# Optimization experiments

Hardware: AMD Instinct MI355X
Metric: run time of the kernel (lower is better)

## Reference

```python
import jax, jax.numpy as jnp
import numpy as np

H = 1024       # hidden_size
V = 32000      # output_vocab_size
STEPS = 375    # fixed greedy decode length in the original loop


def setup_inputs() -> dict:
    key = jax.random.key(0)
    ks = jax.random.split(key, 6)
    s = 0.02  # init scale
    return {
        "encoder_hidden": jax.random.normal(ks[0], (1, 1, H), dtype=jnp.float32),
        "emb": jax.random.normal(ks[1], (V, H), dtype=jnp.float32) * s,
        "W_ih": jax.random.normal(ks[2], (3 * H, H), dtype=jnp.float32) * s,   # [W_ir;W_iz;W_in]
        "W_hh": jax.random.normal(ks[3], (3 * H, H), dtype=jnp.float32) * s,   # [W_hr;W_hz;W_hn]
        "b_ih": jnp.zeros((3 * H,), dtype=jnp.float32),
        "b_hh": jnp.zeros((3 * H,), dtype=jnp.float32),
        "lin_W": jax.random.normal(ks[4], (V, H), dtype=jnp.float32) * s,
        "lin_b": jnp.zeros((V,), dtype=jnp.float32),
    }


def _gru_cell(x, h, W_ih, W_hh, b_ih, b_hh):
    # PyTorch GRU gate math (gate order r, z, n)
    gi = W_ih @ x + b_ih            # [3H]
    gh = W_hh @ h + b_hh            # [3H]
    i_r, i_z, i_n = jnp.split(gi, 3)
    h_r, h_z, h_n = jnp.split(gh, 3)
    r = jax.nn.sigmoid(i_r + h_r)
    z = jax.nn.sigmoid(i_z + h_z)
    n = jnp.tanh(i_n + r * h_n)
    return (1.0 - z) * n + z * h


def reference(encoder_hidden, emb, W_ih, W_hh, b_ih, b_hh, lin_W, lin_b):
    h0 = encoder_hidden[0, 0]  # [H], batch=1, single layer

    def step(carry, _):
        h, tok = carry
        x = emb[tok]                                   # embedding lookup [H]
        h_new = _gru_cell(x, h, W_ih, W_hh, b_ih, b_hh)
        logits = lin_W @ h_new + lin_b                 # [V]
        logp = jax.nn.log_softmax(logits)              # LogSoftmax(dim=1) on [1,V]
        next_tok = jnp.argmax(logp).astype(jnp.int32)  # greedy feedback
        return (h_new, next_tok), logp

    (h_final, _), outs = jax.lax.scan(
        step, (h0, jnp.int32(0)), None, length=STEPS)
    # original cats [1,V] outputs along dim 0 -> [STEPS, V]
    return outs, h_final.reshape(1, 1, H)
```

## Files before the change

kernel.cpp:

```cpp
#include <hip/hip_runtime.h>

#define H 1024
#define V 32000
#define STEPS 375
#define NB1 256
#define NB2 512

typedef float vfloat4 __attribute__((ext_vector_type(4)));

__device__ __forceinline__ float dot4(const float4 a, const float4 b) {
    return fmaf(a.x, b.x, fmaf(a.y, b.y, fmaf(a.z, b.z, a.w * b.w)));
}

__device__ __forceinline__ float wave_sum(float v) {
#pragma unroll
    for (int off = 32; off > 0; off >>= 1) v += __shfl_xor(v, off);
    return v;
}

__device__ __forceinline__ void sm_merge(float& m, float& ss, int& a,
                                         float om, float os, int oa) {
    if (om > m || (om == m && oa < a)) {
        ss = os + ss * expf(m - om); m = om; a = oa;
    } else {
        ss += os * expf(om - m);
    }
}

__device__ __forceinline__ void load_row4(const float4* p, int lane, float4 w[4], bool nt) {
    if (nt) {
        const vfloat4* q = (const vfloat4*)p;
#pragma unroll
        for (int j = 0; j < 4; ++j) {
            vfloat4 t = __builtin_nontemporal_load(&q[lane + 64 * j]);
            w[j] = make_float4(t.x, t.y, t.z, t.w);
        }
    } else {
#pragma unroll
        for (int j = 0; j < 4; ++j) w[j] = p[lane + 64 * j];
    }
}

__global__ void init_kernel(const float* __restrict__ enc, float* __restrict__ h0) {
    for (int i = threadIdx.x; i < H; i += 256) h0[i] = enc[i];
}

__global__ __launch_bounds__(256) void gru_kernel(
    const float* __restrict__ emb, const float* __restrict__ W_ih,
    const float* __restrict__ W_hh, const float* __restrict__ b_ih,
    const float* __restrict__ b_hh, const float* __restrict__ h_cur,
    float* __restrict__ h_next, float* __restrict__ logz,
    const float* __restrict__ pm, const float* __restrict__ ps,
    const int* __restrict__ pa, int s) {
    const int tid = threadIdx.x;
    const int lane = tid & 63;
    const int wv = tid >> 6;
    const int b = blockIdx.x;

    int tok = 0;
    if (s > 0) {
        float m = -3.4e38f, ss = 0.f;
        int a = 0x7fffffff;
#pragma unroll
        for (int k = 0; k < NB2 / 64; ++k)
            sm_merge(m, ss, a, pm[k * 64 + lane], ps[k * 64 + lane], pa[k * 64 + lane]);
#pragma unroll
        for (int off = 32; off > 0; off >>= 1) {
            float om = __shfl_xor(m, off), os = __shfl_xor(ss, off);
            int oa = __shfl_xor(a, off);
            sm_merge(m, ss, a, om, os, oa);
        }
        tok = a;
        if (b == 0 && tid == 0) logz[s - 1] = m + logf(ss);
    }

    const int i = b * 4 + wv;
    const float4* xp = (const float4*)(emb + (size_t)tok * H);
    const float4* hp = (const float4*)h_cur;
    float4 xv[4], hv[4];
#pragma unroll
    for (int j = 0; j < 4; ++j) {
        xv[j] = xp[lane + 64 * j];
        hv[j] = hp[lane + 64 * j];
    }
    float4 WX0[4], WX1[4], WX2[4], WH0[4], WH1[4], WH2[4];
    load_row4((const float4*)(W_ih + (size_t)i * H), lane, WX0, false);
    load_row4((const float4*)(W_ih + ((size_t)i + H) * H), lane, WX1, false);
    load_row4((const float4*)(W_ih + ((size_t)i + 2 * H) * H), lane, WX2, false);
    load_row4((const float4*)(W_hh + (size_t)i * H), lane, WH0, false);
    load_row4((const float4*)(W_hh + ((size_t)i + H) * H), lane, WH1, false);
    load_row4((const float4*)(W_hh + ((size_t)i + 2 * H) * H), lane, WH2, false);
    float sx0 = 0, sx1 = 0, sx2 = 0, sh0 = 0, sh1 = 0, sh2 = 0;
#pragma unroll
    for (int j = 0; j < 4; ++j) {
        sx0 += dot4(WX0[j], xv[j]); sx1 += dot4(WX1[j], xv[j]); sx2 += dot4(WX2[j], xv[j]);
        sh0 += dot4(WH0[j], hv[j]); sh1 += dot4(WH1[j], hv[j]); sh2 += dot4(WH2[j], hv[j]);
    }
    sx0 = wave_sum(sx0); sx1 = wave_sum(sx1); sx2 = wave_sum(sx2);
    sh0 = wave_sum(sh0); sh1 = wave_sum(sh1); sh2 = wave_sum(sh2);
    if (lane == 0) {
        const float rg = 1.f / (1.f + expf(-((sx0 + b_ih[i]) + (sh0 + b_hh[i]))));
        const float zg = 1.f / (1.f + expf(-((sx1 + b_ih[i + H]) + (sh1 + b_hh[i + H]))));
        const float ng = tanhf((sx2 + b_ih[i + 2 * H]) + rg * (sh2 + b_hh[i + 2 * H]));
        h_next[i] = (1.f - zg) * ng + zg * h_cur[i];
    }
}

__global__ __launch_bounds__(512, 4) void logits_kernel(
    const float* __restrict__ lin_W, const float* __restrict__ lin_b,
    const float* __restrict__ h_src, float* __restrict__ orow,
    float* __restrict__ pm, float* __restrict__ ps, int* __restrict__ pa) {
    const int tid = threadIdx.x;
    const int lane = tid & 63;
    const int wv = tid >> 6;
    const int b = blockIdx.x;
    const int row0 = (b < 256) ? 63 * b : 16128 + 62 * (b - 256);
    const int nrows = (b < 256) ? 63 : 62;
    const bool nt = (wv == 3) || (wv == 7);

    __shared__ float red_m[8], red_s[8];
    __shared__ int red_a[8];

    const float4* h4 = (const float4*)h_src;
    float4 hr[4];
#pragma unroll
    for (int j = 0; j < 4; ++j) hr[j] = h4[lane + 64 * j];

    float m = -3.4e38f, ssum = 0.f;
    int arg = 0x7fffffff;
    for (int r = wv; r < nrows; r += 32) {
        const int rB = r + 8, rC = r + 16, rD = r + 24;
        const bool vB = rB < nrows, vC = rC < nrows, vD = rD < nrows;
        float4 wA[4], wB[4], wC[4], wD[4];
        load_row4((const float4*)(lin_W + (size_t)(row0 + r) * H), lane, wA, nt);
        load_row4((const float4*)(lin_W + (size_t)(row0 + (vB ? rB : r)) * H), lane, wB, nt);
        load_row4((const float4*)(lin_W + (size_t)(row0 + (vC ? rC : r)) * H), lane, wC, nt);
        load_row4((const float4*)(lin_W + (size_t)(row0 + (vD ? rD : r)) * H), lane, wD, nt);
        __builtin_amdgcn_sched_barrier(0);
        float aA = 0, aB = 0, aC = 0, aD = 0;
#pragma unroll
        for (int j = 0; j < 4; ++j) {
            aA += dot4(wA[j], hr[j]); aB += dot4(wB[j], hr[j]);
            aC += dot4(wC[j], hr[j]); aD += dot4(wD[j], hr[j]);
        }
        aA = wave_sum(aA); aB = wave_sum(aB);
        aC = wave_sum(aC); aD = wave_sum(aD);
        aA += lin_b[row0 + r];
        if (lane == 0) __builtin_nontemporal_store(aA, &orow[row0 + r]);
        if (aA > m) { ssum *= expf(m - aA); m = aA; arg = row0 + r; }
        ssum += expf(aA - m);
        if (vB) {
            aB += lin_b[row0 + rB];
            if (lane == 0) __builtin_nontemporal_store(aB, &orow[row0 + rB]);
            if (aB > m) { ssum *= expf(m - aB); m = aB; arg = row0 + rB; }
            ssum += expf(aB - m);
        }
        if (vC) {
            aC += lin_b[row0 + rC];
            if (lane == 0) __builtin_nontemporal_store(aC, &orow[row0 + rC]);
            if (aC > m) { ssum *= expf(m - aC); m = aC; arg = row0 + rC; }
            ssum += expf(aC - m);
        }
        if (vD) {
            aD += lin_b[row0 + rD];
            if (lane == 0) __builtin_nontemporal_store(aD, &orow[row0 + rD]);
            if (aD > m) { ssum *= expf(m - aD); m = aD; arg = row0 + rD; }
            ssum += expf(aD - m);
        }
    }
    if (lane == 0) { red_m[wv] = m; red_s[wv] = ssum; red_a[wv] = arg; }
    __syncthreads();
    if (tid == 0) {
        float M = red_m[0], S = red_s[0];
        int A = red_a[0];
#pragma unroll
        for (int w = 1; w < 8; ++w) sm_merge(M, S, A, red_m[w], red_s[w], red_a[w]);
        pm[b] = M; ps[b] = S; pa[b] = A;
    }
}

__global__ __launch_bounds__(256) void final_kernel(float* __restrict__ out,
                                                    const float* __restrict__ logz) {
    const int row = blockIdx.x >> 3;
    const int seg = blockIdx.x & 7;
    const float lz = logz[row];
    float4* p = (float4*)(out + (size_t)row * V) + seg * 1000;
    for (int i = threadIdx.x; i < 1000; i += 256) {
        float4 v = p[i];
        v.x -= lz; v.y -= lz; v.z -= lz; v.w -= lz;
        p[i] = v;
    }
}

__global__ __launch_bounds__(256) void tail_kernel(
    float* __restrict__ out_last, const float* __restrict__ pm,
    const float* __restrict__ ps, const int* __restrict__ pa,
    const float* __restrict__ h_final, float* __restrict__ out_h) {
    const int tid = threadIdx.x;
    const int lane = tid & 63;
    const int b = blockIdx.x;
    float m = -3.4e38f, ss = 0.f;
    int a = 0x7fffffff;
#pragma unroll
    for (int k = 0; k < NB2 / 64; ++k)
        sm_merge(m, ss, a, pm[k * 64 + lane], ps[k * 64 + lane], pa[k * 64 + lane]);
#pragma unroll
    for (int off = 32; off > 0; off >>= 1) {
        float om = __shfl_xor(m, off), os = __shfl_xor(ss, off);
        int oa = __shfl_xor(a, off);
        sm_merge(m, ss, a, om, os, oa);
    }
    const float logZ = m + logf(ss);
    if (tid < 125) out_last[b * 125 + tid] -= logZ;
    if (b == 0)
        for (int i = tid; i < H; i += 256) out_h[i] = h_final[i];
}

extern "C" void kernel_launch(void* const* d_in, const int* in_sizes, int n_in,
                              void* d_out, int out_size, void* d_ws, size_t ws_size,
                              hipStream_t stream) {
    const float* enc = (const float*)d_in[0];
    const float* emb = (const float*)d_in[1];
    const float* W_ih = (const float*)d_in[2];
    const float* W_hh = (const float*)d_in[3];
    const float* b_ih = (const float*)d_in[4];
    const float* b_hh = (const float*)d_in[5];
    const float* lin_W = (const float*)d_in[6];
    const float* lin_b = (const float*)d_in[7];
    float* out = (float*)d_out;
    float* ws = (float*)d_ws;

    float* h_buf = ws;
    float* pm = ws + 2 * H;
    float* ps = pm + NB2;
    int* pa = (int*)(ps + NB2);
    float* logz = (float*)(pa + NB2);

    init_kernel<<<1, 256, 0, stream>>>(enc, h_buf);
    for (int s = 0; s < STEPS; ++s) {
        float* h_cur = h_buf + (s & 1) * H;
        float* h_next = h_buf + ((s + 1) & 1) * H;
        gru_kernel<<<NB1, 256, 0, stream>>>(emb, W_ih, W_hh, b_ih, b_hh,
                                            h_cur, h_next, logz, pm, ps, pa, s);
        logits_kernel<<<NB2, 512, 0, stream>>>(lin_W, lin_b, h_next,
                                               out + (size_t)s * V, pm, ps, pa);
    }
    final_kernel<<<(STEPS - 1) * 8, 256, 0, stream>>>(out, logz);
    tail_kernel<<<NB1, 256, 0, stream>>>(out + (size_t)(STEPS - 1) * V, pm, ps, pa,
                                         h_buf + (STEPS & 1) * H,
                                         out + (size_t)V * STEPS);
}
```

Baseline: 13.02 ms.

## Stream bf16 copy of output projection, recheck near-max rows in fp32

```diff
diff --git a/kernel.cpp b/kernel.cpp
--- a/kernel.cpp
+++ b/kernel.cpp
@@ -5,8 +5,7 @@
 #define STEPS 375
 #define NB1 256
 #define NB2 512
-
-typedef float vfloat4 __attribute__((ext_vector_type(4)));
+#define DELTA 0.25f
 
 __device__ __forceinline__ float dot4(const float4 a, const float4 b) {
     return fmaf(a.x, b.x, fmaf(a.y, b.y, fmaf(a.z, b.z, a.w * b.w)));
@@ -27,22 +26,29 @@
     }
 }
 
-__device__ __forceinline__ void load_row4(const float4* p, int lane, float4 w[4], bool nt) {
-    if (nt) {
-        const vfloat4* q = (const vfloat4*)p;
-#pragma unroll
-        for (int j = 0; j < 4; ++j) {
-            vfloat4 t = __builtin_nontemporal_load(&q[lane + 64 * j]);
-            w[j] = make_float4(t.x, t.y, t.z, t.w);
-        }
-    } else {
-#pragma unroll
-        for (int j = 0; j < 4; ++j) w[j] = p[lane + 64 * j];
-    }
+__device__ __forceinline__ float bl(unsigned u) { return __uint_as_float(u << 16); }
+__device__ __forceinline__ float bh(unsigned u) { return __uint_as_float(u & 0xffff0000u); }
+
+__device__ __forceinline__ unsigned f2bf(float f) {
+    unsigned u = __float_as_uint(f);
+    return (u + 0x7fffu + ((u >> 16) & 1u)) >> 16;
 }
 
 __global__ void init_kernel(const float* __restrict__ enc, float* __restrict__ h0) {
     for (int i = threadIdx.x; i < H; i += 256) h0[i] = enc[i];
+}
+
+__global__ __launch_bounds__(512) void conv_kernel(const float* __restrict__ src,
+                                                   unsigned short* __restrict__ dst) {
+    const size_t idx = (size_t)blockIdx.x * 512 + threadIdx.x;
+    const float4* s4 = (const float4*)src;
+    float4 a = s4[2 * idx], b = s4[2 * idx + 1];
+    uint4 o;
+    o.x = f2bf(a.x) | (f2bf(a.y) << 16);
+    o.y = f2bf(a.z) | (f2bf(a.w) << 16);
+    o.z = f2bf(b.x) | (f2bf(b.y) << 16);
+    o.w = f2bf(b.z) | (f2bf(b.w) << 16);
+    ((uint4*)dst)[idx] = o;
 }
 
 __global__ __launch_bounds__(256) void gru_kernel(
@@ -56,6 +62,22 @@
     const int lane = tid & 63;
     const int wv = tid >> 6;
     const int b = blockIdx.x;
+    const int i = b * 4 + wv;
+
+    const float4* hp = (const float4*)h_cur;
+    float4 hv[4];
+    float4 WX0[4], WX1[4], WX2[4], WH0[4], WH1[4], WH2[4];
+#pragma unroll
+    for (int j = 0; j < 4; ++j) {
+        const int idx = lane + 64 * j;
+        hv[j] = hp[idx];
+        WX0[j] = ((const float4*)(W_ih + (size_t)i * H))[idx];
+        WX1[j] = ((const float4*)(W_ih + ((size_t)i + H) * H))[idx];
+        WX2[j] = ((const float4*)(W_ih + ((size_t)i + 2 * H) * H))[idx];
+        WH0[j] = ((const float4*)(W_hh + (size_t)i * H))[idx];
+        WH1[j] = ((const float4*)(W_hh + ((size_t)i + H) * H))[idx];
+        WH2[j] = ((const float4*)(W_hh + ((size_t)i + 2 * H) * H))[idx];
+    }
 
     int tok = 0;
     if (s > 0) {
@@ -74,22 +96,11 @@
         if (b == 0 && tid == 0) logz[s - 1] = m + logf(ss);
     }
 
-    const int i = b * 4 + wv;
     const float4* xp = (const float4*)(emb + (size_t)tok * H);
-    const float4* hp = (const float4*)h_cur;
-    float4 xv[4], hv[4];
-#pragma unroll
-    for (int j = 0; j < 4; ++j) {
-        xv[j] = xp[lane + 64 * j];
-        hv[j] = hp[lane + 64 * j];
-    }
-    float4 WX0[4], WX1[4], WX2[4], WH0[4], WH1[4], WH2[4];
-    load_row4((const float4*)(W_ih + (size_t)i * H), lane, WX0, false);
-    load_row4((const float4*)(W_ih + ((size_t)i + H) * H), lane, WX1, false);
-    load_row4((const float4*)(W_ih + ((size_t)i + 2 * H) * H), lane, WX2, false);
-    load_row4((const float4*)(W_hh + (size_t)i * H), lane, WH0, false);
-    load_row4((const float4*)(W_hh + ((size_t)i + H) * H), lane, WH1, false);
-    load_row4((const float4*)(W_hh + ((size_t)i + 2 * H) * H), lane, WH2, false);
+    float4 xv[4];
+#pragma unroll
+    for (int j = 0; j < 4; ++j) xv[j] = xp[lane + 64 * j];
+
     float sx0 = 0, sx1 = 0, sx2 = 0, sh0 = 0, sh1 = 0, sh2 = 0;
 #pragma unroll
     for (int j = 0; j < 4; ++j) {
@@ -106,7 +117,120 @@
     }
 }
 
-__global__ __launch_bounds__(512, 4) void logits_kernel(
+__global__ __launch_bounds__(512, 4) void logits_bf16_kernel(
+    const unsigned short* __restrict__ wbf, const float* __restrict__ lin_W,
+    const float* __restrict__ lin_b, const float* __restrict__ h_src,
+    float* __restrict__ orow, float* __restrict__ pm, float* __restrict__ ps,
+    int* __restrict__ pa) {
+    const int tid = threadIdx.x;
+    const int lane = tid & 63;
+    const int wv = tid >> 6;
+    const int b = blockIdx.x;
+    const int row0 = (b < 256) ? 63 * b : 16128 + 62 * (b - 256);
+    const int nrows = (b < 256) ? 63 : 62;
+
+    __shared__ float red_m[8], red_s[8];
+    __shared__ float s_cm[8];
+    __shared__ int s_ca[8];
+
+    const float4* h4 = (const float4*)h_src;
+    const float4 ha0 = h4[2 * lane], ha1 = h4[2 * lane + 1];
+    const float4 hb0 = h4[128 + 2 * lane], hb1 = h4[129 + 2 * lane];
+    const float h0[8] = {ha0.x, ha0.y, ha0.z, ha0.w, ha1.x, ha1.y, ha1.z, ha1.w};
+    const float h1[8] = {hb0.x, hb0.y, hb0.z, hb0.w, hb1.x, hb1.y, hb1.z, hb1.w};
+
+    float lg[8];
+    float m = -3.4e38f, ssum = 0.f;
+
+#pragma unroll
+    for (int half = 0; half < 2; ++half) {
+        const int k0 = half * 4;
+        uint4 qa[4], qb[4];
+        int rr[4];
+        bool val[4];
+#pragma unroll
+        for (int i2 = 0; i2 < 4; ++i2) {
+            rr[i2] = wv + 8 * (k0 + i2);
+            val[i2] = rr[i2] < nrows;
+            const uint4* wp = (const uint4*)(wbf + (size_t)(row0 + (val[i2] ? rr[i2] : 0)) * H);
+            qa[i2] = wp[lane];
+            qb[i2] = wp[64 + lane];
+        }
+        __builtin_amdgcn_sched_barrier(0);
+#pragma unroll
+        for (int i2 = 0; i2 < 4; ++i2) {
+            float a = 0.f;
+            a = fmaf(bl(qa[i2].x), h0[0], a); a = fmaf(bh(qa[i2].x), h0[1], a);
+            a = fmaf(bl(qa[i2].y), h0[2], a); a = fmaf(bh(qa[i2].y), h0[3], a);
+            a = fmaf(bl(qa[i2].z), h0[4], a); a = fmaf(bh(qa[i2].z), h0[5], a);
+            a = fmaf(bl(qa[i2].w), h0[6], a); a = fmaf(bh(qa[i2].w), h0[7], a);
+            a = fmaf(bl(qb[i2].x), h1[0], a); a = fmaf(bh(qb[i2].x), h1[1], a);
+            a = fmaf(bl(qb[i2].y), h1[2], a); a = fmaf(bh(qb[i2].y), h1[3], a);
+            a = fmaf(bl(qb[i2].z), h1[4], a); a = fmaf(bh(qb[i2].z), h1[5], a);
+            a = fmaf(bl(qb[i2].w), h1[6], a); a = fmaf(bh(qb[i2].w), h1[7], a);
+            a = wave_sum(a);
+            if (val[i2]) {
+                const int col = row0 + rr[i2];
+                a += lin_b[col];
+                lg[k0 + i2] = a;
+                if (lane == 0) __builtin_nontemporal_store(a, &orow[col]);
+                if (a > m) { ssum *= expf(m - a); m = a; }
+                ssum += expf(a - m);
+            } else {
+                lg[k0 + i2] = -3.4e38f;
+            }
+        }
+    }
+    if (lane == 0) { red_m[wv] = m; red_s[wv] = ssum; }
+    __syncthreads();
+
+    float Mb = red_m[0];
+#pragma unroll
+    for (int w = 1; w < 8; ++w) Mb = fmaxf(Mb, red_m[w]);
+
+    float cm = -3.4e38f;
+    int ca = 0x7fffffff;
+    float4 hv[4];
+    bool loaded = false;
+#pragma unroll
+    for (int k = 0; k < 8; ++k) {
+        if (lg[k] > Mb - DELTA) {
+            const int row = row0 + wv + 8 * k;
+            if (!loaded) {
+#pragma unroll
+                for (int j = 0; j < 4; ++j) hv[j] = h4[lane + 64 * j];
+                loaded = true;
+            }
+            const float4* rp = (const float4*)(lin_W + (size_t)row * H);
+            float a = 0.f;
+#pragma unroll
+            for (int j = 0; j < 4; ++j) a += dot4(rp[lane + 64 * j], hv[j]);
+            a = wave_sum(a) + lin_b[row];
+            if (a > cm || (a == cm && row < ca)) { cm = a; ca = row; }
+        }
+    }
+    if (lane == 0) { s_cm[wv] = cm; s_ca[wv] = ca; }
+    __syncthreads();
+    if (tid == 0) {
+        float M = red_m[0], S = red_s[0];
+#pragma unroll
+        for (int w = 1; w < 8; ++w) {
+            const float mw = red_m[w], sw = red_s[w];
+            if (mw > M) { S = sw + S * expf(M - mw); M = mw; }
+            else S += sw * expf(mw - M);
+        }
+        float CM = s_cm[0];
+        int CA = s_ca[0];
+#pragma unroll
+        for (int w = 1; w < 8; ++w)
+            if (s_cm[w] > CM || (s_cm[w] == CM && s_ca[w] < CA)) { CM = s_cm[w]; CA = s_ca[w]; }
+        pm[b] = CM;
+        ps[b] = S * expf(M - CM);
+        pa[b] = CA;
+    }
+}
+
+__global__ __launch_bounds__(512, 4) void logits_fp32_kernel(
     const float* __restrict__ lin_W, const float* __restrict__ lin_b,
     const float* __restrict__ h_src, float* __restrict__ orow,
     float* __restrict__ pm, float* __restrict__ ps, int* __restrict__ pa) {
@@ -116,7 +240,6 @@
     const int b = blockIdx.x;
     const int row0 = (b < 256) ? 63 * b : 16128 + 62 * (b - 256);
     const int nrows = (b < 256) ? 63 : 62;
-    const bool nt = (wv == 3) || (wv == 7);
 
     __shared__ float red_m[8], red_s[8];
     __shared__ int red_a[8];
@@ -132,10 +255,14 @@
         const int rB = r + 8, rC = r + 16, rD = r + 24;
         const bool vB = rB < nrows, vC = rC < nrows, vD = rD < nrows;
         float4 wA[4], wB[4], wC[4], wD[4];
-        load_row4((const float4*)(lin_W + (size_t)(row0 + r) * H), lane, wA, nt);
-        load_row4((const float4*)(lin_W + (size_t)(row0 + (vB ? rB : r)) * H), lane, wB, nt);
-        load_row4((const float4*)(lin_W + (size_t)(row0 + (vC ? rC : r)) * H), lane, wC, nt);
-        load_row4((const float4*)(lin_W + (size_t)(row0 + (vD ? rD : r)) * H), lane, wD, nt);
+#pragma unroll
+        for (int j = 0; j < 4; ++j) {
+            const int idx = lane + 64 * j;
+            wA[j] = ((const float4*)(lin_W + (size_t)(row0 + r) * H))[idx];
+            wB[j] = ((const float4*)(lin_W + (size_t)(row0 + (vB ? rB : r)) * H))[idx];
+            wC[j] = ((const float4*)(lin_W + (size_t)(row0 + (vC ? rC : r)) * H))[idx];
+            wD[j] = ((const float4*)(lin_W + (size_t)(row0 + (vD ? rD : r)) * H))[idx];
+        }
         __builtin_amdgcn_sched_barrier(0);
         float aA = 0, aB = 0, aC = 0, aD = 0;
 #pragma unroll
@@ -235,15 +362,24 @@
     float* ps = pm + NB2;
     int* pa = (int*)(ps + NB2);
     float* logz = (float*)(pa + NB2);
+    unsigned short* wbf = (unsigned short*)((char*)d_ws + 16384);
+    const size_t need = 16384 + (size_t)V * H * 2;
+    const bool bf16path = ws_size >= need;
 
     init_kernel<<<1, 256, 0, stream>>>(enc, h_buf);
+    if (bf16path)
+        conv_kernel<<<V * H / 8 / 512, 512, 0, stream>>>(lin_W, wbf);
     for (int s = 0; s < STEPS; ++s) {
         float* h_cur = h_buf + (s & 1) * H;
         float* h_next = h_buf + ((s + 1) & 1) * H;
         gru_kernel<<<NB1, 256, 0, stream>>>(emb, W_ih, W_hh, b_ih, b_hh,
                                             h_cur, h_next, logz, pm, ps, pa, s);
-        logits_kernel<<<NB2, 512, 0, stream>>>(lin_W, lin_b, h_next,
-                                               out + (size_t)s * V, pm, ps, pa);
+        if (bf16path)
+            logits_bf16_kernel<<<NB2, 512, 0, stream>>>(wbf, lin_W, lin_b, h_next,
+                                                        out + (size_t)s * V, pm, ps, pa);
+        else
+            logits_fp32_kernel<<<NB2, 512, 0, stream>>>(lin_W, lin_b, h_next,
+                                                        out + (size_t)s * V, pm, ps, pa);
     }
     final_kernel<<<(STEPS - 1) * 8, 256, 0, stream>>>(out, logz);
     tail_kernel<<<NB1, 256, 0, stream>>>(out + (size_t)(STEPS - 1) * V, pm, ps, pa,
```

New measurement: 15.55 ms. +19.5%, slower.
